# Kernel tuning notes

Hardware: AMD Instinct MI355X
Metric: run time of the kernel (lower is better)

Reference implementation:

```python
import jax, jax.numpy as jnp
import numpy as np
from jax import lax
from jax.scipy.special import logsumexp

B, L, D = 8, 2048, 1330  # esm_dim=1280 + 50
H1, H2, T = 32, 16, 2


def setup_inputs() -> dict:
    key = jax.random.key(0)
    ks = jax.random.split(key, 12)
    x = jax.random.normal(ks[0], (B, L, D), jnp.float32)
    tokens_length = jax.random.randint(ks[1], (B,), 1, L + 1)
    labels = jax.random.randint(ks[2], (B, L), 0, T)
    s = 0.05
    w1 = jax.random.normal(ks[3], (D, H1), jnp.float32) * s
    b1 = jnp.zeros((H1,), jnp.float32)
    conv_w = jax.random.normal(ks[4], (H2, H1, 3), jnp.float32) * s  # OIH
    conv_b = jnp.zeros((H2,), jnp.float32)
    w2 = jax.random.normal(ks[5], (H2, T), jnp.float32) * s
    b2 = jnp.zeros((T,), jnp.float32)
    start_trans = jax.random.normal(ks[6], (T,), jnp.float32) * 0.1
    end_trans = jax.random.normal(ks[7], (T,), jnp.float32) * 0.1
    trans = jax.random.normal(ks[8], (T, T), jnp.float32) * 0.1
    return {"x": x, "tokens_length": tokens_length, "labels": labels,
            "w1": w1, "b1": b1, "conv_w": conv_w, "conv_b": conv_b,
            "w2": w2, "b2": b2, "start_trans": start_trans,
            "end_trans": end_trans, "trans": trans}


def _emission(x, w1, b1, conv_w, conv_b, w2, b2):
    h = x @ w1 + b1                       # [B,L,32] (dropout off: eval)
    h = jnp.transpose(h, (0, 2, 1))       # [B,32,L]
    h = lax.conv_general_dilated(h, conv_w, (1,), [(1, 1)],
                                 dimension_numbers=("NCH", "OIH", "NCH"))
    h = jax.nn.relu(h + conv_b[None, :, None])
    h = jnp.transpose(h, (0, 2, 1))       # [B,L,16]
    return h @ w2 + b2                    # [B,L,2]


def reference(x, tokens_length, labels, w1, b1, conv_w, conv_b, w2, b2,
              start_trans, end_trans, trans):
    em = _emission(x, w1, b1, conv_w, conv_b, w2, b2)    # [B,L,T]
    mask = jnp.arange(L)[None, :] < tokens_length[:, None]  # [B,L] bool

    emT = jnp.transpose(em, (1, 0, 2))   # [L,B,T]
    maskT = mask.T                        # [L,B]
    labT = labels.T                       # [L,B]
    bidx = jnp.arange(B)

    # ---- gold path score (torchcrf _compute_score) ----
    s0 = start_trans[labT[0]] + emT[0][bidx, labT[0]]

    def score_step(carry, inp):
        s, prev = carry
        em_i, lab_i, m_i = inp
        add = trans[prev, lab_i] + jnp.take_along_axis(em_i, lab_i[:, None], axis=1)[:, 0]
        s = s + jnp.where(m_i, add, 0.0)
        prev = jnp.where(m_i, lab_i, prev)
        return (s, prev), None

    (score, _), _ = lax.scan(score_step, (s0, labT[0]),
                             (emT[1:], labT[1:], maskT[1:]))
    seq_ends = tokens_length - 1
    last_tags = labels[bidx, seq_ends]
    score = score + end_trans[last_tags]

    # ---- log-partition (forward algorithm) ----
    a0 = start_trans[None, :] + emT[0]    # [B,T]

    def norm_step(a, inp):
        em_i, m_i = inp
        nxt = logsumexp(a[:, :, None] + trans[None, :, :] + em_i[:, None, :], axis=1)
        return jnp.where(m_i[:, None], nxt, a), None

    a, _ = lax.scan(norm_step, a0, (emT[1:], maskT[1:]))
    norm = logsumexp(a + end_trans[None, :], axis=1)

    llh = score - norm
    neg_loss = -jnp.sum(llh)              # module returns -crf(...), reduction='sum'

    # ---- Viterbi decode ----
    v0 = start_trans[None, :] + emT[0]
    ident = jnp.broadcast_to(jnp.arange(T)[None, :], (B, T))

    def vit_step(v, inp):
        em_i, m_i = inp
        scores = v[:, :, None] + trans[None, :, :]      # [B,prev,cur]
        idx = jnp.argmax(scores, axis=1)                # [B,T]
        best = jnp.max(scores, axis=1) + em_i
        v_new = jnp.where(m_i[:, None], best, v)
        idx = jnp.where(m_i[:, None], idx, ident)       # identity on padded steps
        return v_new, idx

    v, hist = lax.scan(vit_step, v0, (emT[1:], maskT[1:]))  # hist: [L-1,B,T]
    last = jnp.argmax(v + end_trans[None, :], axis=1)       # [B]

    def back_step(tag, h_t):
        prev = jnp.take_along_axis(h_t, tag[:, None], axis=1)[:, 0]
        return prev, prev

    _, tags_front = lax.scan(back_step, last, hist, reverse=True)  # [L-1,B]
    tags = jnp.concatenate([tags_front, last[None, :]], axis=0).T  # [B,L]
    tags = jnp.where(mask, tags, 0)

    return neg_loss, tags


if __name__ == "__main__":
    out = reference(**setup_inputs())
    print(out[0], out[1].shape)
```

## Files before the change

kernel.cpp:

```cpp
#include <hip/hip_runtime.h>

#define LSEQ 2048
#define DIN  1330
#define NB   8
#define SPLITK 7
#define KCH 192
#define K1PAD 1344
#define NSTEP 6

typedef short bf16x8 __attribute__((ext_vector_type(8)));
typedef float f32x4  __attribute__((ext_vector_type(4)));
typedef unsigned short ushort8v __attribute__((ext_vector_type(8)));

__device__ __forceinline__ float lsef(float a, float b) {
  float m = fmaxf(a, b);
  float d = fminf(a, b) - m;
  return m + log1pf(__expf(d));
}

__device__ __forceinline__ unsigned short f2bf(float f) {
  unsigned int u = __float_as_uint(f);
  return (unsigned short)((u + 0x7FFFu + ((u >> 16) & 1u)) >> 16);
}

__global__ __launch_bounds__(256) void k0_wt(
    const float* __restrict__ w1, unsigned short* __restrict__ w1T) {
  const int f = (blockIdx.x * 256 + threadIdx.x) * 4;
  const int h = f / K1PAD, k = f % K1PAD;
  ushort4 v;
  v.x = (k     < DIN) ? f2bf(w1[(long)(k)     * 32 + h]) : (unsigned short)0;
  v.y = (k + 1 < DIN) ? f2bf(w1[(long)(k + 1) * 32 + h]) : (unsigned short)0;
  v.z = (k + 2 < DIN) ? f2bf(w1[(long)(k + 2) * 32 + h]) : (unsigned short)0;
  v.w = (k + 3 < DIN) ? f2bf(w1[(long)(k + 3) * 32 + h]) : (unsigned short)0;
  *(ushort4*)(w1T + f) = v;
}

__global__ __launch_bounds__(256) void k1_mfma(
    const float* __restrict__ x, const unsigned short* __restrict__ w1T,
    float* __restrict__ p) {
  __shared__ unsigned short smem[2 * 2560 + 2 * 1280];

  const int tid = threadIdx.x;
  const int rb  = blockIdx.x / SPLITK;
  const int s   = blockIdx.x % SPLITK;
  const int k0  = s * KCH;
  const long row0 = (long)rb * 64;

  const int arow = tid >> 2;
  const int ako  = (tid & 3) * 8;
  const float* ap = x + (row0 + arow) * DIN;
  const int bh   = tid >> 3;
  const int bk4  = (tid & 7) * 4;

  const int wid  = tid >> 6;
  const int lane = tid & 63;
  const int fr   = lane & 15;
  const int fg   = lane >> 4;

  f32x4 acc0 = {0.f, 0.f, 0.f, 0.f};
  f32x4 acc1 = {0.f, 0.f, 0.f, 0.f};

  float4 aCur0, aCur1, aNxt0, aNxt1;
  ushort4 bCur, bNxt;

  auto stage_load = [&](int tt, float4& a0, float4& a1, ushort4& bv) {
    const int ka = k0 + tt * 32 + ako;
    float4 u = make_float4(0.f, 0.f, 0.f, 0.f);
    float4 v = make_float4(0.f, 0.f, 0.f, 0.f);
    if (ka + 7 < DIN) {
      u = *(const float4*)(ap + ka);
      v = *(const float4*)(ap + ka + 4);
    } else {
      if (ka     < DIN) u.x = ap[ka];
      if (ka + 1 < DIN) u.y = ap[ka + 1];
      if (ka + 2 < DIN) u.z = ap[ka + 2];
      if (ka + 3 < DIN) u.w = ap[ka + 3];
      if (ka + 4 < DIN) v.x = ap[ka + 4];
      if (ka + 5 < DIN) v.y = ap[ka + 5];
      if (ka + 6 < DIN) v.z = ap[ka + 6];
      if (ka + 7 < DIN) v.w = ap[ka + 7];
    }
    a0 = u; a1 = v;
    bv = *(const ushort4*)(w1T + (long)bh * K1PAD + k0 + tt * 32 + bk4);
  };

  auto stage_write = [&](int bi, const float4& a0, const float4& a1, const ushort4& bv) {
    ushort8v apk;
    apk[0] = f2bf(a0.x); apk[1] = f2bf(a0.y); apk[2] = f2bf(a0.z); apk[3] = f2bf(a0.w);
    apk[4] = f2bf(a1.x); apk[5] = f2bf(a1.y); apk[6] = f2bf(a1.z); apk[7] = f2bf(a1.w);
    *(ushort8v*)(smem + bi * 2560 + arow * 40 + ako) = apk;
    *(ushort4*)(smem + 5120 + bi * 1280 + bh * 40 + bk4) = bv;
  };

  stage_load(0, aCur0, aCur1, bCur);

  #pragma unroll 1
  for (int t = 0; t < NSTEP; ++t) {
    stage_write(t & 1, aCur0, aCur1, bCur);
    if (t + 1 < NSTEP) stage_load(t + 1, aNxt0, aNxt1, bNxt);
    __syncthreads();

    const unsigned short* sa = smem + (t & 1) * 2560;
    const unsigned short* sb = smem + 5120 + (t & 1) * 1280;
    const bf16x8 a  = *(const bf16x8*)(sa + (wid * 16 + fr) * 40 + fg * 8);
    const bf16x8 b0 = *(const bf16x8*)(sb + fr * 40 + fg * 8);
    const bf16x8 b1 = *(const bf16x8*)(sb + (16 + fr) * 40 + fg * 8);
    acc0 = __builtin_amdgcn_mfma_f32_16x16x32_bf16(a, b0, acc0, 0, 0, 0);
    acc1 = __builtin_amdgcn_mfma_f32_16x16x32_bf16(a, b1, acc1, 0, 0, 0);

    aCur0 = aNxt0; aCur1 = aNxt1; bCur = bNxt;
  }

  float* ps = p + (long)s * 524288 + (row0 + wid * 16 + fg * 4) * 32;
  #pragma unroll
  for (int i = 0; i < 4; ++i) {
    ps[(long)i * 32 + fr]      = acc0[i];
    ps[(long)i * 32 + 16 + fr] = acc1[i];
  }
}

__global__ __launch_bounds__(256) void k2_conv(
    const float* __restrict__ p, const float* __restrict__ b1,
    const float* __restrict__ cw, const float* __restrict__ cb,
    const float* __restrict__ w2, const float* __restrict__ b2,
    float* __restrict__ em) {
  const int g = blockIdx.x * 256 + threadIdx.x;
  const int row  = g >> 3;
  const int isub = g & 7;
  const int i0   = isub << 2;
  const int li   = row & (LSEQ - 1);

  const float4* p4 = (const float4*)p;
  const float4 bv = ((const float4*)b1)[isub];
  float4 z; z.x = z.y = z.z = z.w = 0.f;

  auto hrow = [&](int r) -> float4 {
    float4 a = p4[(long)r * 8 + isub];
    #pragma unroll
    for (int s = 1; s < SPLITK; ++s) {
      float4 v = p4[(long)s * 131072 + (long)r * 8 + isub];
      a.x += v.x; a.y += v.y; a.z += v.z; a.w += v.w;
    }
    a.x += bv.x; a.y += bv.y; a.z += bv.z; a.w += bv.w;
    return a;
  };

  float4 hm = (li > 0)        ? hrow(row - 1) : z;
  float4 hc = hrow(row);
  float4 hp = (li < LSEQ - 1) ? hrow(row + 1) : z;

  float s[16];
  #pragma unroll
  for (int o = 0; o < 16; ++o) {
    const float4* wpq = (const float4*)(cw + o * 96 + i0 * 3);
    const float4 wa = wpq[0], wb = wpq[1], wc = wpq[2];
    s[o] = hm.x * wa.x + hc.x * wa.y + hp.x * wa.z
         + hm.y * wa.w + hc.y * wb.x + hp.y * wb.y
         + hm.z * wb.z + hc.z * wb.w + hp.z * wc.x
         + hm.w * wc.y + hc.w * wc.z + hp.w * wc.w;
  }
  #pragma unroll
  for (int o = 0; o < 16; ++o) {
    s[o] += __shfl_xor(s[o], 1, 8);
    s[o] += __shfl_xor(s[o], 2, 8);
    s[o] += __shfl_xor(s[o], 4, 8);
  }
  if (isub == 0) {
    float e0 = b2[0], e1 = b2[1];
    #pragma unroll
    for (int o = 0; o < 16; ++o) {
      float rr = fmaxf(s[o] + cb[o], 0.f);
      e0 += rr * w2[o * 2];
      e1 += rr * w2[o * 2 + 1];
    }
    float2 ev; ev.x = e0; ev.y = e1;
    *(float2*)(em + (long)row * 2) = ev;
  }
}

__global__ __launch_bounds__(256) void k3_crf(
    const float* __restrict__ em, const int* __restrict__ tokens_length,
    const int* __restrict__ labels, const float* __restrict__ start_trans,
    const float* __restrict__ end_trans, const float* __restrict__ trans,
    float* __restrict__ llh, float* __restrict__ out) {
  __shared__ float sem[LSEQ * 2];
  __shared__ unsigned char hist[LSEQ];
  __shared__ float4 mats[256];
  __shared__ float red[256];
  __shared__ unsigned char bmA[256], bmB[256];
  __shared__ int s_last;

  const int t = threadIdx.x;
  const int b = blockIdx.x & 7;
  const int role = blockIdx.x >> 3;
  const int len = tokens_length[b];
  const float t00 = trans[0], t01 = trans[1], t10 = trans[2], t11 = trans[3];
  const float st0 = start_trans[0], st1 = start_trans[1];
  const float en0 = end_trans[0], en1 = end_trans[1];
  const int* lab = labels + b * LSEQ;

  {
    const float4* src4 = (const float4*)(em + (long)b * LSEQ * 2);
    float4* dst4 = (float4*)sem;
    #pragma unroll
    for (int i = t; i < LSEQ * 2 / 4; i += 256) dst4[i] = src4[i];
    if (role == 1) {
      #pragma unroll
      for (int l = t; l < LSEQ; l += 256) hist[l] = 2;
    }
  }
  __syncthreads();

  int lo = t * 8; if (lo < 1) lo = 1;
  int hi = t * 8 + 8; if (hi > len) hi = len;

  if (role == 0) {
    float sc = 0.f;
    {
      const int base = t * 8;
      #pragma unroll
      for (int k = 0; k < 8; ++k) {
        int l = base + k;
        if (l >= 1 && l < len) {
          int lp = lab[l - 1], lc = lab[l];
          sc += trans[lp * 2 + lc] + sem[2 * l + lc];
        }
      }
    }
    red[t] = sc;

    {
      float p00 = 0.f, p01 = -1e30f, p10 = -1e30f, p11 = 0.f;
      for (int l = lo; l < hi; ++l) {
        float e0 = sem[2 * l], e1 = sem[2 * l + 1];
        float n00 = lsef(p00 + t00, p01 + t10) + e0;
        float n01 = lsef(p00 + t01, p01 + t11) + e1;
        float n10 = lsef(p10 + t00, p11 + t10) + e0;
        float n11 = lsef(p10 + t01, p11 + t11) + e1;
        p00 = n00; p01 = n01; p10 = n10; p11 = n11;
      }
      float4 m; m.x = p00; m.y = p01; m.z = p10; m.w = p11; mats[t] = m;
    }
    __syncthreads();

    for (int n = 128; n >= 1; n >>= 1) {
      if (t < n) red[t] += red[t + n];
      __syncthreads();
    }
    for (int n = 128; n >= 1; n >>= 1) {
      float4 A, B; const bool act = (t < n);
      if (act) { A = mats[2 * t]; B = mats[2 * t + 1]; }
      __syncthreads();
      if (act) {
        float4 C;
        C.x = lsef(A.x + B.x, A.y + B.z);
        C.y = lsef(A.x + B.y, A.y + B.w);
        C.z = lsef(A.z + B.x, A.w + B.z);
        C.w = lsef(A.z + B.y, A.w + B.w);
        mats[t] = C;
      }
      __syncthreads();
    }

    if (t == 0) {
      int lab0 = lab[0];
      float s0 = (lab0 ? st1 : st0) + sem[lab0];
      int labe = lab[len - 1];
      float score = red[0] + s0 + (labe ? en1 : en0);
      float4 M = mats[0];
      float a00 = st0 + sem[0], a01 = st1 + sem[1];
      float af0 = lsef(a00 + M.x, a01 + M.z);
      float af1 = lsef(a00 + M.y, a01 + M.w);
      float norm = lsef(af0 + en0, af1 + en1);
      llh[b] = score - norm;
    }
    return;
  }

  {
    float q00 = 0.f, q01 = -1e30f, q10 = -1e30f, q11 = 0.f;
    for (int l = lo; l < hi; ++l) {
      float e0 = sem[2 * l], e1 = sem[2 * l + 1];
      float n00 = fmaxf(q00 + t00, q01 + t10) + e0;
      float n01 = fmaxf(q00 + t01, q01 + t11) + e1;
      float n10 = fmaxf(q10 + t00, q11 + t10) + e0;
      float n11 = fmaxf(q10 + t01, q11 + t11) + e1;
      q00 = n00; q01 = n01; q10 = n10; q11 = n11;
    }
    float4 m; m.x = q00; m.y = q01; m.z = q10; m.w = q11; mats[t] = m;
  }
  __syncthreads();

  for (int off = 1; off < 256; off <<= 1) {
    float4 cur = mats[t];
    float4 prv;
    const bool has = (t >= off);
    if (has) prv = mats[t - off];
    __syncthreads();
    if (has) {
      float4 c;
      c.x = fmaxf(prv.x + cur.x, prv.y + cur.z);
      c.y = fmaxf(prv.x + cur.y, prv.y + cur.w);
      c.z = fmaxf(prv.z + cur.x, prv.w + cur.z);
      c.w = fmaxf(prv.z + cur.y, prv.w + cur.w);
      mats[t] = c;
    }
    __syncthreads();
  }

  {
    const float v00 = st0 + sem[0], v01 = st1 + sem[1];
    float vp0, vp1;
    if (t == 0) { vp0 = v00; vp1 = v01; }
    else {
      float4 E = mats[t - 1];
      vp0 = fmaxf(v00 + E.x, v01 + E.z);
      vp1 = fmaxf(v00 + E.y, v01 + E.w);
    }
    for (int l = lo; l < hi; ++l) {
      float e0 = sem[2 * l], e1 = sem[2 * l + 1];
      float s00 = vp0 + t00, s10 = vp1 + t10;
      float s01 = vp0 + t01, s11 = vp1 + t11;
      hist[l] = (unsigned char)((s00 >= s10 ? 0 : 1) | ((s01 >= s11 ? 0 : 1) << 1));
      vp0 = fmaxf(s00, s10) + e0;
      vp1 = fmaxf(s01, s11) + e1;
    }
    if (hi == len && lo < hi)
      s_last = (vp0 + en0 >= vp1 + en1) ? 0 : 1;
    if (t == 0 && len == 1)
      s_last = (v00 + en0 >= v01 + en1) ? 0 : 1;
  }
  __syncthreads();
  const int last = s_last;

  {
    int blo = (t == 0) ? 1 : t * 8;
    int bhi = t * 8 + 8;
    int m0 = 0, m1 = 1;
    for (int l = bhi - 1; l >= blo; --l) {
      int h = hist[l];
      m0 = (h >> m0) & 1;
      m1 = (h >> m1) & 1;
    }
    bmA[t] = (unsigned char)(m0 | (m1 << 1));
  }
  __syncthreads();
  {
    unsigned char* sarr = bmA; unsigned char* darr = bmB;
    for (int off = 1; off < 256; off <<= 1) {
      int a = sarr[t];
      int c = a;
      if (t + off < 256) {
        int bm = sarr[t + off];
        int c0 = (a >> (bm & 1)) & 1;
        int c1 = (a >> ((bm >> 1) & 1)) & 1;
        c = c0 | (c1 << 1);
      }
      darr[t] = (unsigned char)c;
      __syncthreads();
      unsigned char* tmp = sarr; sarr = darr; darr = tmp;
    }
    int xv = (t == 255) ? last : ((sarr[t + 1] >> last) & 1);
    int blo = (t == 0) ? 1 : t * 8;
    int bhi = t * 8 + 8;
    float* tout = out + 1 + b * LSEQ;
    for (int l = bhi - 1; l >= blo; --l) {
      xv = (hist[l] >> xv) & 1;
      int pidx = l - 1;
      tout[pidx] = (pidx < len) ? (float)xv : 0.0f;
    }
    if (t == 255) tout[LSEQ - 1] = ((LSEQ - 1) < len) ? (float)last : 0.0f;
  }
}

__global__ void k4_final(const float* __restrict__ llh, float* __restrict__ out) {
  if (threadIdx.x == 0 && blockIdx.x == 0) {
    float s = 0.f;
    #pragma unroll
    for (int i = 0; i < NB; ++i) s += llh[i];
    out[0] = -s;
  }
}

extern "C" void kernel_launch(void* const* d_in, const int* in_sizes, int n_in,
                              void* d_out, int out_size, void* d_ws, size_t ws_size,
                              hipStream_t stream) {
  const float* x  = (const float*)d_in[0];
  const int*   tl = (const int*)d_in[1];
  const int*   lb = (const int*)d_in[2];
  const float* w1 = (const float*)d_in[3];
  const float* b1 = (const float*)d_in[4];
  const float* cw = (const float*)d_in[5];
  const float* cb = (const float*)d_in[6];
  const float* w2 = (const float*)d_in[7];
  const float* b2 = (const float*)d_in[8];
  const float* st = (const float*)d_in[9];
  const float* en = (const float*)d_in[10];
  const float* tr = (const float*)d_in[11];
  float* out = (float*)d_out;
  float* ws  = (float*)d_ws;

  float* p   = ws;
  float* em  = ws + (long)SPLITK * 524288;
  float* llh = em + 32768;
  unsigned short* w1T = (unsigned short*)(llh + 16);

  hipLaunchKernelGGL(k0_wt, dim3(42), dim3(256), 0, stream, w1, w1T);
  hipLaunchKernelGGL(k1_mfma, dim3(256 * SPLITK), dim3(256), 0, stream, x, w1T, p);
  hipLaunchKernelGGL(k2_conv, dim3(512), dim3(256), 0, stream, p, b1, cw, cb, w2, b2, em);
  hipLaunchKernelGGL(k3_crf, dim3(16), dim3(256), 0, stream, em, tl, lb, st, en, tr, llh, out);
  hipLaunchKernelGGL(k4_final, dim3(1), dim3(64), 0, stream, llh, out);
}
```

Before: 58.20 us.

## Load MFMA operands directly from global memory, dropping the LDS staging and barriers

The split-K bf16 MFMA GEMM kernel no longer stages A and B tiles through double-buffered shared memory with __syncthreads. Each lane now loads its own fragment of x (fp32, converted to bf16 in registers) and of w1T straight from global memory, and the six K-steps are fully unrolled. This removes the LDS writes and reads and the block barriers, and lets the compiler issue all loads early. In exchange, each lane reads 32-byte strided row segments, so global coalescing is less regular, and the B tile is loaded redundantly by every wave, leaning on the cache.

```diff
diff --git a/kernel.cpp b/kernel.cpp
--- a/kernel.cpp
+++ b/kernel.cpp
@@ -10,7 +10,6 @@
 
 typedef short bf16x8 __attribute__((ext_vector_type(8)));
 typedef float f32x4  __attribute__((ext_vector_type(4)));
-typedef unsigned short ushort8v __attribute__((ext_vector_type(8)));
 
 __device__ __forceinline__ float lsef(float a, float b) {
   float m = fmaxf(a, b);
@@ -38,39 +37,34 @@
 __global__ __launch_bounds__(256) void k1_mfma(
     const float* __restrict__ x, const unsigned short* __restrict__ w1T,
     float* __restrict__ p) {
-  __shared__ unsigned short smem[2 * 2560 + 2 * 1280];
-
-  const int tid = threadIdx.x;
-  const int rb  = blockIdx.x / SPLITK;
-  const int s   = blockIdx.x % SPLITK;
-  const int k0  = s * KCH;
-  const long row0 = (long)rb * 64;
-
-  const int arow = tid >> 2;
-  const int ako  = (tid & 3) * 8;
-  const float* ap = x + (row0 + arow) * DIN;
-  const int bh   = tid >> 3;
-  const int bk4  = (tid & 7) * 4;
-
-  const int wid  = tid >> 6;
+  const int tid  = threadIdx.x;
+  const int rb   = blockIdx.x / SPLITK;
+  const int s    = blockIdx.x % SPLITK;
+  const int k0   = s * KCH;
+
+  const int wv   = tid >> 6;
   const int lane = tid & 63;
   const int fr   = lane & 15;
   const int fg   = lane >> 4;
 
+  const long row  = (long)rb * 64 + wv * 16 + fr;
+  const float* ap = x + row * DIN;
+  const unsigned short* bp0 = w1T + (long)fr * K1PAD;
+  const unsigned short* bp1 = w1T + (long)(16 + fr) * K1PAD;
+
   f32x4 acc0 = {0.f, 0.f, 0.f, 0.f};
   f32x4 acc1 = {0.f, 0.f, 0.f, 0.f};
 
-  float4 aCur0, aCur1, aNxt0, aNxt1;
-  ushort4 bCur, bNxt;
-
-  auto stage_load = [&](int tt, float4& a0, float4& a1, ushort4& bv) {
-    const int ka = k0 + tt * 32 + ako;
-    float4 u = make_float4(0.f, 0.f, 0.f, 0.f);
-    float4 v = make_float4(0.f, 0.f, 0.f, 0.f);
+  #pragma unroll
+  for (int t = 0; t < NSTEP; ++t) {
+    const int ka = k0 + t * 32 + fg * 8;
+    float4 u, v;
     if (ka + 7 < DIN) {
       u = *(const float4*)(ap + ka);
       v = *(const float4*)(ap + ka + 4);
     } else {
+      u = make_float4(0.f, 0.f, 0.f, 0.f);
+      v = make_float4(0.f, 0.f, 0.f, 0.f);
       if (ka     < DIN) u.x = ap[ka];
       if (ka + 1 < DIN) u.y = ap[ka + 1];
       if (ka + 2 < DIN) u.z = ap[ka + 2];
@@ -80,38 +74,20 @@
       if (ka + 6 < DIN) v.z = ap[ka + 6];
       if (ka + 7 < DIN) v.w = ap[ka + 7];
     }
-    a0 = u; a1 = v;
-    bv = *(const ushort4*)(w1T + (long)bh * K1PAD + k0 + tt * 32 + bk4);
-  };
-
-  auto stage_write = [&](int bi, const float4& a0, const float4& a1, const ushort4& bv) {
-    ushort8v apk;
-    apk[0] = f2bf(a0.x); apk[1] = f2bf(a0.y); apk[2] = f2bf(a0.z); apk[3] = f2bf(a0.w);
-    apk[4] = f2bf(a1.x); apk[5] = f2bf(a1.y); apk[6] = f2bf(a1.z); apk[7] = f2bf(a1.w);
-    *(ushort8v*)(smem + bi * 2560 + arow * 40 + ako) = apk;
-    *(ushort4*)(smem + 5120 + bi * 1280 + bh * 40 + bk4) = bv;
-  };
-
-  stage_load(0, aCur0, aCur1, bCur);
-
-  #pragma unroll 1
-  for (int t = 0; t < NSTEP; ++t) {
-    stage_write(t & 1, aCur0, aCur1, bCur);
-    if (t + 1 < NSTEP) stage_load(t + 1, aNxt0, aNxt1, bNxt);
-    __syncthreads();
-
-    const unsigned short* sa = smem + (t & 1) * 2560;
-    const unsigned short* sb = smem + 5120 + (t & 1) * 1280;
-    const bf16x8 a  = *(const bf16x8*)(sa + (wid * 16 + fr) * 40 + fg * 8);
-    const bf16x8 b0 = *(const bf16x8*)(sb + fr * 40 + fg * 8);
-    const bf16x8 b1 = *(const bf16x8*)(sb + (16 + fr) * 40 + fg * 8);
+    bf16x8 a;
+    a[0] = (short)f2bf(u.x); a[1] = (short)f2bf(u.y);
+    a[2] = (short)f2bf(u.z); a[3] = (short)f2bf(u.w);
+    a[4] = (short)f2bf(v.x); a[5] = (short)f2bf(v.y);
+    a[6] = (short)f2bf(v.z); a[7] = (short)f2bf(v.w);
+
+    const bf16x8 b0 = *(const bf16x8*)(bp0 + ka);
+    const bf16x8 b1 = *(const bf16x8*)(bp1 + ka);
+
     acc0 = __builtin_amdgcn_mfma_f32_16x16x32_bf16(a, b0, acc0, 0, 0, 0);
     acc1 = __builtin_amdgcn_mfma_f32_16x16x32_bf16(a, b1, acc1, 0, 0, 0);
-
-    aCur0 = aNxt0; aCur1 = aNxt1; bCur = bNxt;
-  }
-
-  float* ps = p + (long)s * 524288 + (row0 + wid * 16 + fg * 4) * 32;
+  }
+
+  float* ps = p + (long)s * 524288 + ((long)rb * 64 + wv * 16 + fg * 4) * 32;
   #pragma unroll
   for (int i = 0; i < 4; ++i) {
     ps[(long)i * 32 + fr]      = acc0[i];
```

Result: no change. 59.34 us (+2.0%).
